# Kernel optimization log

Measured on AMD Instinct MI355X. Metric: run time of the kernel, lower is better.

The kernel has to match this reference:

```python
import jax, jax.numpy as jnp
import numpy as np

B, L, D_MODEL, N_HEADS = 2, 2048, 2048, 16
HALF = D_MODEL // 2            # 1024
HD = HALF // N_HEADS           # 64 (head dim actually used by the reshape)
SCALE = float(np.sqrt(D_MODEL / N_HEADS))  # sqrt(128), per source's self.scale
EPS = 1e-5


def setup_inputs() -> dict:
    key = jax.random.key(0)
    ks = jax.random.split(key, 12)
    s = 1.0 / np.sqrt(HALF)
    d = dict(
        x_a=jax.random.normal(ks[0], (B, L, HALF), jnp.float32),
        x_b=jax.random.normal(ks[1], (B, L, HALF), jnp.float32),
        Wq_a=jax.random.normal(ks[2], (HALF, HALF), jnp.float32) * s,
        Wq_b=jax.random.normal(ks[3], (HALF, HALF), jnp.float32) * s,
        Wk_a=jax.random.normal(ks[4], (HALF, HALF), jnp.float32) * s,
        Wk_b=jax.random.normal(ks[5], (HALF, HALF), jnp.float32) * s,
        Wv_a=jax.random.normal(ks[6], (HALF, HALF), jnp.float32) * s,
        Wv_b=jax.random.normal(ks[7], (HALF, HALF), jnp.float32) * s,
        Wo_a=jax.random.normal(ks[8], (HALF, HALF), jnp.float32) * s,
        Wo_b=jax.random.normal(ks[9], (HALF, HALF), jnp.float32) * s,
        gamma_a=jnp.ones((HALF,), jnp.float32),
        beta_a=jnp.zeros((HALF,), jnp.float32),
        gamma_b=jnp.ones((HALF,), jnp.float32),
        beta_b=jnp.zeros((HALF,), jnp.float32),
    )
    return d


def _heads(x, W):
    # torch Linear (no bias): x @ W.T, then split heads -> (B, H, L, HD)
    y = jnp.einsum('bld,ed->ble', x, W)
    Bb, Ll, _ = y.shape
    return y.reshape(Bb, Ll, N_HEADS, HD).transpose(0, 2, 1, 3)


def _ln(x, gamma, beta):
    mu = jnp.mean(x, axis=-1, keepdims=True)
    var = jnp.var(x, axis=-1, keepdims=True)
    return (x - mu) * jax.lax.rsqrt(var + EPS) * gamma + beta


def reference(x_a, x_b, Wq_a, Wq_b, Wk_a, Wk_b, Wv_a, Wv_b, Wo_a, Wo_b,
              gamma_a, beta_a, gamma_b, beta_b):
    q_a = _heads(x_a, Wq_a); k_a = _heads(x_a, Wk_a); v_a = _heads(x_a, Wv_a)
    q_b = _heads(x_b, Wq_b); k_b = _heads(x_b, Wk_b); v_b = _heads(x_b, Wv_b)

    # cross-attention: branch a attends over branch b and vice versa
    scores_a = jnp.einsum('bhqd,bhkd->bhqk', q_a, k_b) / SCALE
    scores_b = jnp.einsum('bhqd,bhkd->bhqk', q_b, k_a) / SCALE
    w_a = jax.nn.softmax(scores_a, axis=-1)
    w_b = jax.nn.softmax(scores_b, axis=-1)

    o_a = jnp.einsum('bhqk,bhkd->bhqd', w_a, v_b)
    o_b = jnp.einsum('bhqk,bhkd->bhqd', w_b, v_a)
    o_a = o_a.transpose(0, 2, 1, 3).reshape(x_a.shape)
    o_b = o_b.transpose(0, 2, 1, 3).reshape(x_b.shape)

    o_a = jnp.einsum('bld,ed->ble', o_a, Wo_a)
    o_b = jnp.einsum('bld,ed->ble', o_b, Wo_b)

    y_a = _ln(x_a + o_a, gamma_a, beta_a)
    y_b = _ln(x_b + o_b, gamma_b, beta_b)
    return y_a, y_b
```

## Files before the change

### kernel.cpp

```cpp
#include <hip/hip_runtime.h>
#include <cstdint>
#include <cstddef>

typedef __bf16 bf16x8 __attribute__((ext_vector_type(8)));
typedef float f32x4 __attribute__((ext_vector_type(4)));
typedef unsigned short u16x8 __attribute__((ext_vector_type(8)));
typedef unsigned short u16x4 __attribute__((ext_vector_type(4)));
typedef short s16x4 __attribute__((ext_vector_type(4)));
typedef unsigned short u16;

#define L_SEQ 2048
#define D_HALF 1024
#define HDIM 64
static constexpr float EXP2_SCALE = 0.12751742552639395f;

__device__ inline u16 f2b(float f) {
  uint32_t u; __builtin_memcpy(&u, &f, 4);
  u = u + 0x7FFFu + ((u >> 16) & 1u);
  return (u16)(u >> 16);
}

__device__ inline uint32_t cvt_pk_bf16(float lo, float hi) {
  uint32_t r;
  asm("v_cvt_pk_bf16_f32 %0, %1, %2" : "=v"(r) : "v"(lo), "v"(hi));
  return r;
}

#define GLOAD16(gp, lp) __builtin_amdgcn_global_load_lds( \
    (const __attribute__((address_space(1))) unsigned int*)(gp), \
    (__attribute__((address_space(3))) unsigned int*)(lp), 16, 0, 0)

struct CArgAll { const float* src[10]; u16* dst[10]; };
__global__ __launch_bounds__(256)
void convall(CArgAll a) {
  const int id = blockIdx.x;
  const float* s; u16* d; int blk;
  if (id < 4096) { int p = id >> 11; blk = id & 2047; s = a.src[p]; d = a.dst[p]; }
  else { int w = (id - 4096) >> 9; blk = (id - 4096) & 511; s = a.src[2 + w]; d = a.dst[2 + w]; }
  size_t i = ((size_t)blk * 256 + threadIdx.x) * 8;
  float4 v0 = *(const float4*)(s + i);
  float4 v1 = *(const float4*)(s + i + 4);
  u16x8 p;
  p[0] = f2b(v0.x); p[1] = f2b(v0.y); p[2] = f2b(v0.z); p[3] = f2b(v0.w);
  p[4] = f2b(v1.x); p[5] = f2b(v1.y); p[6] = f2b(v1.z); p[7] = f2b(v1.w);
  *(u16x8*)&d[i] = p;
}

struct GArg { const u16* A; const u16* W; u16* C; const float* R; float* Z;
              int vt; float alpha; };
struct GArgs { GArg g[6]; };

template <bool RESID>
__global__ __launch_bounds__(256)
void gemm_nt(GArgs args, int M, int N, int K) {
  GArg ga = args.g[blockIdx.z];
  __shared__ __attribute__((aligned(16))) u16 As[2][8192];
  __shared__ __attribute__((aligned(16))) u16 Bs[2][8192];

  const int tid = threadIdx.x;
  const int wv = tid >> 6, lane = tid & 63;
  const int lane15 = lane & 15, quad = lane >> 4;
  const int m0 = blockIdx.y * 128, n0 = blockIdx.x * 128;
  const int wm = (wv >> 1) * 64, wn = (wv & 1) * 64;

  const int srow = lane >> 3;
  const int scol = ((lane & 7) ^ srow) * 8;

  const u16* pA[4]; const u16* pW[4]; int lo[4];
#pragma unroll
  for (int j = 0; j < 4; j++) {
    int r = wv * 32 + j * 8;
    pA[j] = ga.A + (size_t)(m0 + r + srow) * K + scol;
    pW[j] = ga.W + (size_t)(n0 + r + srow) * K + scol;
    lo[j] = r * 64;
  }

  f32x4 acc[4][4] = {};
  const int swz = (lane15 & 7) << 4;
  const int NT = K >> 6;

#pragma unroll
  for (int j = 0; j < 4; j++) {
    GLOAD16(pA[j], &As[0][lo[j]]);
    GLOAD16(pW[j], &Bs[0][lo[j]]);
  }
#pragma unroll
  for (int j = 0; j < 4; j++) {
    GLOAD16(pA[j] + 64, &As[1][lo[j]]);
    GLOAD16(pW[j] + 64, &Bs[1][lo[j]]);
  }
  asm volatile("s_waitcnt vmcnt(8)" ::: "memory");
  __builtin_amdgcn_s_barrier();
  __builtin_amdgcn_sched_barrier(0);

  for (int t = 0; t < NT; ++t) {
    const int cur = t & 1;
    const char* ab = (const char*)As[cur];
    const char* bb = (const char*)Bs[cur];
#pragma unroll
    for (int kk = 0; kk < 2; kk++) {
      const int cb = kk * 64 + quad * 16;
      bf16x8 af[4], bw[4];
#pragma unroll
      for (int i = 0; i < 4; i++)
        af[i] = *(const bf16x8*)(ab + (wm + i * 16 + lane15) * 128 + (cb ^ swz));
#pragma unroll
      for (int j = 0; j < 4; j++)
        bw[j] = *(const bf16x8*)(bb + (wn + j * 16 + lane15) * 128 + (cb ^ swz));
#pragma unroll
      for (int i = 0; i < 4; i++)
#pragma unroll
        for (int j = 0; j < 4; j++)
          acc[i][j] = __builtin_amdgcn_mfma_f32_16x16x32_bf16(af[i], bw[j], acc[i][j], 0, 0, 0);
    }
    __builtin_amdgcn_sched_barrier(0);
    __builtin_amdgcn_s_barrier();
    __builtin_amdgcn_sched_barrier(0);
    if (t + 2 < NT) {
#pragma unroll
      for (int j = 0; j < 4; j++) {
        GLOAD16(pA[j] + (size_t)(t + 2) * 64, &As[cur][lo[j]]);
        GLOAD16(pW[j] + (size_t)(t + 2) * 64, &Bs[cur][lo[j]]);
      }
      asm volatile("s_waitcnt vmcnt(8)" ::: "memory");
    } else if (t + 1 < NT) {
      asm volatile("s_waitcnt vmcnt(0)" ::: "memory");
    }
    if (t + 1 < NT) {
      __builtin_amdgcn_s_barrier();
      __builtin_amdgcn_sched_barrier(0);
    }
  }

  const float al = ga.alpha;
  if (!RESID && ga.vt) {
#pragma unroll
    for (int i = 0; i < 4; i++)
#pragma unroll
      for (int j = 0; j < 4; j++) {
        int gm0 = m0 + wm + i * 16 + quad * 4;
        int gn  = n0 + wn + j * 16 + lane15;
        int bb2 = gm0 >> 11, tt = gm0 & 2047;
        u16x4 pk;
#pragma unroll
        for (int r = 0; r < 4; r++) pk[r] = f2b(acc[i][j][r] * al);
        *(u16x4*)&ga.C[(size_t)bb2 * 2097152 + (size_t)gn * 2048 + tt] = pk;
      }
  } else {
#pragma unroll
    for (int i = 0; i < 4; i++)
#pragma unroll
      for (int j = 0; j < 4; j++)
#pragma unroll
        for (int r = 0; r < 4; r++) {
          int gm = m0 + wm + i * 16 + quad * 4 + r;
          int gn = n0 + wn + j * 16 + lane15;
          size_t idx = (size_t)gm * N + gn;
          if (RESID) ga.Z[idx] = acc[i][j][r] + ga.R[idx];
          else       ga.C[idx] = f2b(acc[i][j][r] * al);
        }
  }
}

#define SWZ(row, bcol) ((row) * 128 + ((bcol) ^ (((row) & 7) << 4)))

__global__ __launch_bounds__(256, 2)
void attn_kernel(const u16* q_a, const u16* k_a, const u16* vt_a,
                 const u16* q_b, const u16* k_b, const u16* vt_b,
                 u16* o_a, u16* o_b) {
  const int br = blockIdx.z;
  const u16* Q  = br ? q_b : q_a;
  const u16* Kp = br ? k_a : k_b;
  const u16* Vp = br ? vt_a : vt_b;
  u16* O = br ? o_b : o_a;
  const int bh = blockIdx.y;
  const int b = bh >> 4, h = bh & 15;
  const int q0 = blockIdx.x * 128;

  const int tid = threadIdx.x, wv = tid >> 6, lane = tid & 63;
  const int lane15 = lane & 15, quad = lane >> 4;

  __shared__ __attribute__((aligned(16))) u16 Ks[2][4096];
  __shared__ __attribute__((aligned(16))) u16 Vt[2][4096];

  const size_t base   = ((size_t)b * L_SEQ) * D_HALF + (size_t)h * HDIM;
  const size_t vbase  = (size_t)b * 2097152 + (size_t)(h * 64) * 2048;

  const int c1 = tid + 256;
  const int r0 = tid >> 3, cb0 = (tid & 7) * 16;
  const int r1 = c1 >> 3,  cb1 = (c1 & 7) * 16;
  const int wo0 = SWZ(r0, cb0), wo1 = SWZ(r1, cb1);

  bf16x8 qf[2][2];
#pragma unroll
  for (int f = 0; f < 2; f++) {
    const int qrow = q0 + wv * 32 + f * 16 + lane15;
#pragma unroll
    for (int c = 0; c < 2; c++)
      qf[f][c] = *(const bf16x8*)&Q[base + (size_t)qrow * D_HALF + c * 32 + quad * 8];
  }

  u16x8 kr0 = *(const u16x8*)&Kp[base + (size_t)r0 * D_HALF + cb0 / 2];
  u16x8 kr1 = *(const u16x8*)&Kp[base + (size_t)r1 * D_HALF + cb1 / 2];
  u16x8 vr0 = *(const u16x8*)&Vp[vbase + (size_t)r0 * 2048 + cb0 / 2];
  u16x8 vr1 = *(const u16x8*)&Vp[vbase + (size_t)r1 * 2048 + cb1 / 2];
  *(u16x8*)((char*)Ks[0] + wo0) = kr0;
  *(u16x8*)((char*)Ks[0] + wo1) = kr1;
  *(u16x8*)((char*)Vt[0] + wo0) = vr0;
  *(u16x8*)((char*)Vt[0] + wo1) = vr1;
  __syncthreads();

  f32x4 oacc[2][4] = {};
  float lsum[2] = {0.f, 0.f};

  for (int it = 0; it < 32; it++) {
    const int cur = it & 1, nxt = cur ^ 1;
    if (it < 31) {
      const int kt = (it + 1) * 64;
      kr0 = *(const u16x8*)&Kp[base + (size_t)(kt + r0) * D_HALF + cb0 / 2];
      kr1 = *(const u16x8*)&Kp[base + (size_t)(kt + r1) * D_HALF + cb1 / 2];
      vr0 = *(const u16x8*)&Vp[vbase + (size_t)r0 * 2048 + kt + cb0 / 2];
      vr1 = *(const u16x8*)&Vp[vbase + (size_t)r1 * 2048 + kt + cb1 / 2];
    }

    const char* kb = (const char*)Ks[cur];
    const char* vb = (const char*)Vt[cur];

    f32x4 s[2][4];
    __builtin_amdgcn_s_setprio(1);
#pragma unroll
    for (int nt = 0; nt < 4; nt++) {
      const int krow = nt * 16 + lane15;
      bf16x8 kb0 = *(const bf16x8*)(kb + SWZ(krow, quad * 16));
      bf16x8 kb1 = *(const bf16x8*)(kb + SWZ(krow, 64 + quad * 16));
#pragma unroll
      for (int f = 0; f < 2; f++) {
        f32x4 a0 = {};
        a0 = __builtin_amdgcn_mfma_f32_16x16x32_bf16(kb0, qf[f][0], a0, 0, 0, 0);
        a0 = __builtin_amdgcn_mfma_f32_16x16x32_bf16(kb1, qf[f][1], a0, 0, 0, 0);
        s[f][nt] = a0;
      }
    }
    __builtin_amdgcn_s_setprio(0);

    s16x4 pa[2][4];
#pragma unroll
    for (int f = 0; f < 2; f++)
#pragma unroll
      for (int nt = 0; nt < 4; nt++) {
        float p0 = __builtin_amdgcn_exp2f(s[f][nt][0]);
        float p1 = __builtin_amdgcn_exp2f(s[f][nt][1]);
        float p2 = __builtin_amdgcn_exp2f(s[f][nt][2]);
        float p3 = __builtin_amdgcn_exp2f(s[f][nt][3]);
        lsum[f] += (p0 + p1) + (p2 + p3);
        union { uint32_t u[2]; s16x4 v; } cv;
        cv.u[0] = cvt_pk_bf16(p0, p1);
        cv.u[1] = cvt_pk_bf16(p2, p3);
        pa[f][nt] = cv.v;
      }

    __builtin_amdgcn_s_setprio(1);
#pragma unroll
    for (int dt = 0; dt < 4; dt++) {
      const int vrow = dt * 16 + lane15;
      s16x4 bv[4];
#pragma unroll
      for (int nt = 0; nt < 4; nt++)
        bv[nt] = *(const s16x4*)(vb + SWZ(vrow, nt * 32 + quad * 8));
#pragma unroll
      for (int f = 0; f < 2; f++) {
        f32x4 t = oacc[f][dt];
#pragma unroll
        for (int nt = 0; nt < 4; nt++)
          t = __builtin_amdgcn_mfma_f32_16x16x16bf16_1k(pa[f][nt], bv[nt], t, 0, 0, 0);
        oacc[f][dt] = t;
      }
    }
    __builtin_amdgcn_s_setprio(0);

    if (it < 31) {
      *(u16x8*)((char*)Ks[nxt] + wo0) = kr0;
      *(u16x8*)((char*)Ks[nxt] + wo1) = kr1;
      *(u16x8*)((char*)Vt[nxt] + wo0) = vr0;
      *(u16x8*)((char*)Vt[nxt] + wo1) = vr1;
    }
    __syncthreads();
  }

#pragma unroll
  for (int f = 0; f < 2; f++) {
    float lt = lsum[f];
    lt += __shfl_xor(lt, 16);
    lt += __shfl_xor(lt, 32);
    lsum[f] = lt;
  }
#pragma unroll
  for (int f = 0; f < 2; f++) {
    float linv[4];
#pragma unroll
    for (int r = 0; r < 4; r++)
      linv[r] = 1.0f / __shfl(lsum[f], quad * 4 + r);
#pragma unroll
    for (int dt = 0; dt < 4; dt++)
#pragma unroll
      for (int r = 0; r < 4; r++) {
        float val = oacc[f][dt][r] * linv[r];
        O[base + (size_t)(q0 + wv * 32 + f * 16 + quad * 4 + r) * D_HALF
          + dt * 16 + lane15] = f2b(val);
      }
  }
}

__global__ __launch_bounds__(256)
void ln_kernel(const float* zA, const float* zB,
               const float* gA, const float* bA, const float* gB, const float* bB,
               float* out) {
  const int row = blockIdx.x, br = blockIdx.y;
  const float* z = (br ? zB : zA) + (size_t)row * D_HALF;
  const float* g  = br ? gB : gA;
  const float* be = br ? bB : bA;
  float* o = out + (size_t)br * ((size_t)4096 * D_HALF) + (size_t)row * D_HALF;

  float4 v = ((const float4*)z)[threadIdx.x];
  float s  = v.x + v.y + v.z + v.w;
  float s2 = v.x * v.x + v.y * v.y + v.z * v.z + v.w * v.w;
#pragma unroll
  for (int off = 32; off > 0; off >>= 1) {
    s  += __shfl_down(s, off);
    s2 += __shfl_down(s2, off);
  }
  __shared__ float red[8];
  int w = threadIdx.x >> 6, ln = threadIdx.x & 63;
  if (ln == 0) { red[w] = s; red[4 + w] = s2; }
  __syncthreads();
  if (threadIdx.x == 0) {
    red[0] = red[0] + red[1] + red[2] + red[3];
    red[4] = red[4] + red[5] + red[6] + red[7];
  }
  __syncthreads();
  float mu  = red[0] * (1.0f / 1024.0f);
  float var = red[4] * (1.0f / 1024.0f) - mu * mu;
  float rs  = rsqrtf(fmaxf(var, 0.0f) + 1e-5f);

  int col = threadIdx.x * 4;
  float4 gv = ((const float4*)g)[threadIdx.x];
  float4 bv = ((const float4*)be)[threadIdx.x];
  float4 ov;
  ov.x = (v.x - mu) * rs * gv.x + bv.x;
  ov.y = (v.y - mu) * rs * gv.y + bv.y;
  ov.z = (v.z - mu) * rs * gv.z + bv.z;
  ov.w = (v.w - mu) * rs * gv.w + bv.w;
  *(float4*)&o[col] = ov;
}

extern "C" void kernel_launch(void* const* d_in, const int* in_sizes, int n_in,
                              void* d_out, int out_size, void* d_ws, size_t ws_size,
                              hipStream_t stream) {
  const float* x_a     = (const float*)d_in[0];
  const float* x_b     = (const float*)d_in[1];
  const float* Wq_a    = (const float*)d_in[2];
  const float* Wq_b    = (const float*)d_in[3];
  const float* Wk_a    = (const float*)d_in[4];
  const float* Wk_b    = (const float*)d_in[5];
  const float* Wv_a    = (const float*)d_in[6];
  const float* Wv_b    = (const float*)d_in[7];
  const float* Wo_a    = (const float*)d_in[8];
  const float* Wo_b    = (const float*)d_in[9];
  const float* gamma_a = (const float*)d_in[10];
  const float* beta_a  = (const float*)d_in[11];
  const float* gamma_b = (const float*)d_in[12];
  const float* beta_b  = (const float*)d_in[13];

  const size_t BUF = (size_t)4096 * 1024;
  u16* ws   = (u16*)d_ws;
  u16* q_a  = ws + 0 * BUF; u16* k_a  = ws + 1 * BUF; u16* vt_a = ws + 2 * BUF;
  u16* q_b  = ws + 3 * BUF; u16* k_b  = ws + 4 * BUF; u16* vt_b = ws + 5 * BUF;
  u16* wall = ws + 6 * BUF;
  float* z_a = (float*)(ws + 0 * BUF);
  float* z_b = (float*)(ws + 2 * BUF);

  u16* xbf_a = (u16*)d_out;
  u16* xbf_b = xbf_a + 4194304;
  u16* o_a   = (u16*)d_out;
  u16* o_b   = o_a + 4194304;

  const int M = 4096, N = 1024, K = 1024;

  CArgAll ca;
  ca.src[0] = x_a;  ca.dst[0] = xbf_a;
  ca.src[1] = x_b;  ca.dst[1] = xbf_b;
  ca.src[2] = Wq_a; ca.src[3] = Wk_a; ca.src[4] = Wv_a;
  ca.src[5] = Wq_b; ca.src[6] = Wk_b; ca.src[7] = Wv_b;
  ca.src[8] = Wo_a; ca.src[9] = Wo_b;
  for (int w = 0; w < 8; w++) ca.dst[2 + w] = wall + (size_t)w * 1048576;
  convall<<<dim3(8192), 256, 0, stream>>>(ca);

  GArgs qkv;
  qkv.g[0] = GArg{xbf_a, wall + 0 * 1048576, q_a,  nullptr, nullptr, 0, EXP2_SCALE};
  qkv.g[1] = GArg{xbf_a, wall + 1 * 1048576, k_a,  nullptr, nullptr, 0, 1.0f};
  qkv.g[2] = GArg{xbf_a, wall + 2 * 1048576, vt_a, nullptr, nullptr, 1, 1.0f};
  qkv.g[3] = GArg{xbf_b, wall + 3 * 1048576, q_b,  nullptr, nullptr, 0, EXP2_SCALE};
  qkv.g[4] = GArg{xbf_b, wall + 4 * 1048576, k_b,  nullptr, nullptr, 0, 1.0f};
  qkv.g[5] = GArg{xbf_b, wall + 5 * 1048576, vt_b, nullptr, nullptr, 1, 1.0f};
  gemm_nt<false><<<dim3(8, 32, 6), 256, 0, stream>>>(qkv, M, N, K);

  attn_kernel<<<dim3(16, 32, 2), 256, 0, stream>>>(q_a, k_a, vt_a, q_b, k_b, vt_b, o_a, o_b);

  GArgs op;
  op.g[0] = GArg{o_a, wall + 6 * 1048576, nullptr, x_a, z_a, 0, 1.0f};
  op.g[1] = GArg{o_b, wall + 7 * 1048576, nullptr, x_b, z_b, 0, 1.0f};
  op.g[2] = op.g[0]; op.g[3] = op.g[0]; op.g[4] = op.g[0]; op.g[5] = op.g[0];
  gemm_nt<true><<<dim3(8, 32, 2), 256, 0, stream>>>(op, M, N, K);

  ln_kernel<<<dim3(4096, 2), 256, 0, stream>>>(z_a, z_b, gamma_a, beta_a,
                                               gamma_b, beta_b, (float*)d_out);
}
```

Measured before the change: 342.0 us.

## Single-buffer GEMM LDS and remap 1D grid with XCD-aware block swizzle

Replaces the hand-scheduled double-buffered LDS pipeline in the NT GEMM with a simple single-buffer load/sync/compute loop. This halves LDS use so more workgroups can fit per CU. It also flattens the launch grid to 1D and remaps block ids so consecutive ids land on the same XCD, interleaving the GEMM sub-problems (z) for better L2 locality. The cost is that global loads no longer overlap with MFMA compute, so each k-step now waits for its loads behind two barriers.

```diff
diff --git a/kernel.cpp b/kernel.cpp
--- a/kernel.cpp
+++ b/kernel.cpp
@@ -52,15 +52,23 @@
 
 template <bool RESID>
 __global__ __launch_bounds__(256)
-void gemm_nt(GArgs args, int M, int N, int K) {
-  GArg ga = args.g[blockIdx.z];
-  __shared__ __attribute__((aligned(16))) u16 As[2][8192];
-  __shared__ __attribute__((aligned(16))) u16 Bs[2][8192];
+void gemm_nt(GArgs args, int N, int K, int ZN) {
+  const int nwg = gridDim.x;
+  const int q8 = nwg >> 3;
+  const int bid = ((int)blockIdx.x & 7) * q8 + ((int)blockIdx.x >> 3);
+  const int z = bid % ZN;
+  const int rem = bid / ZN;
+  const int nx = N >> 7;
+  const int bx = rem % nx, by = rem / nx;
+
+  GArg ga = args.g[z];
+  __shared__ __attribute__((aligned(16))) u16 As[8192];
+  __shared__ __attribute__((aligned(16))) u16 Bs[8192];
 
   const int tid = threadIdx.x;
   const int wv = tid >> 6, lane = tid & 63;
   const int lane15 = lane & 15, quad = lane >> 4;
-  const int m0 = blockIdx.y * 128, n0 = blockIdx.x * 128;
+  const int m0 = by * 128, n0 = bx * 128;
   const int wm = (wv >> 1) * 64, wn = (wv & 1) * 64;
 
   const int srow = lane >> 3;
@@ -77,26 +85,17 @@
 
   f32x4 acc[4][4] = {};
   const int swz = (lane15 & 7) << 4;
-  const int NT = K >> 6;
-
-#pragma unroll
-  for (int j = 0; j < 4; j++) {
-    GLOAD16(pA[j], &As[0][lo[j]]);
-    GLOAD16(pW[j], &Bs[0][lo[j]]);
-  }
-#pragma unroll
-  for (int j = 0; j < 4; j++) {
-    GLOAD16(pA[j] + 64, &As[1][lo[j]]);
-    GLOAD16(pW[j] + 64, &Bs[1][lo[j]]);
-  }
-  asm volatile("s_waitcnt vmcnt(8)" ::: "memory");
-  __builtin_amdgcn_s_barrier();
-  __builtin_amdgcn_sched_barrier(0);
-
-  for (int t = 0; t < NT; ++t) {
-    const int cur = t & 1;
-    const char* ab = (const char*)As[cur];
-    const char* bb = (const char*)Bs[cur];
+
+  for (int k0 = 0; k0 < K; k0 += 64) {
+    __syncthreads();
+#pragma unroll
+    for (int j = 0; j < 4; j++) {
+      GLOAD16(pA[j] + k0, &As[lo[j]]);
+      GLOAD16(pW[j] + k0, &Bs[lo[j]]);
+    }
+    __syncthreads();
+    const char* ab = (const char*)As;
+    const char* bb = (const char*)Bs;
 #pragma unroll
     for (int kk = 0; kk < 2; kk++) {
       const int cb = kk * 64 + quad * 16;
@@ -112,23 +111,6 @@
 #pragma unroll
         for (int j = 0; j < 4; j++)
           acc[i][j] = __builtin_amdgcn_mfma_f32_16x16x32_bf16(af[i], bw[j], acc[i][j], 0, 0, 0);
-    }
-    __builtin_amdgcn_sched_barrier(0);
-    __builtin_amdgcn_s_barrier();
-    __builtin_amdgcn_sched_barrier(0);
-    if (t + 2 < NT) {
-#pragma unroll
-      for (int j = 0; j < 4; j++) {
-        GLOAD16(pA[j] + (size_t)(t + 2) * 64, &As[cur][lo[j]]);
-        GLOAD16(pW[j] + (size_t)(t + 2) * 64, &Bs[cur][lo[j]]);
-      }
-      asm volatile("s_waitcnt vmcnt(8)" ::: "memory");
-    } else if (t + 1 < NT) {
-      asm volatile("s_waitcnt vmcnt(0)" ::: "memory");
-    }
-    if (t + 1 < NT) {
-      __builtin_amdgcn_s_barrier();
-      __builtin_amdgcn_sched_barrier(0);
     }
   }
 
@@ -384,7 +366,7 @@
   u16* o_a   = (u16*)d_out;
   u16* o_b   = o_a + 4194304;
 
-  const int M = 4096, N = 1024, K = 1024;
+  const int N = 1024, K = 1024;
 
   CArgAll ca;
   ca.src[0] = x_a;  ca.dst[0] = xbf_a;
@@ -402,7 +384,7 @@
   qkv.g[3] = GArg{xbf_b, wall + 3 * 1048576, q_b,  nullptr, nullptr, 0, EXP2_SCALE};
   qkv.g[4] = GArg{xbf_b, wall + 4 * 1048576, k_b,  nullptr, nullptr, 0, 1.0f};
   qkv.g[5] = GArg{xbf_b, wall + 5 * 1048576, vt_b, nullptr, nullptr, 1, 1.0f};
-  gemm_nt<false><<<dim3(8, 32, 6), 256, 0, stream>>>(qkv, M, N, K);
+  gemm_nt<false><<<dim3(8 * 32 * 6), 256, 0, stream>>>(qkv, N, K, 6);
 
   attn_kernel<<<dim3(16, 32, 2), 256, 0, stream>>>(q_a, k_a, vt_a, q_b, k_b, vt_b, o_a, o_b);
 
@@ -410,7 +392,7 @@
   op.g[0] = GArg{o_a, wall + 6 * 1048576, nullptr, x_a, z_a, 0, 1.0f};
   op.g[1] = GArg{o_b, wall + 7 * 1048576, nullptr, x_b, z_b, 0, 1.0f};
   op.g[2] = op.g[0]; op.g[3] = op.g[0]; op.g[4] = op.g[0]; op.g[5] = op.g[0];
-  gemm_nt<true><<<dim3(8, 32, 2), 256, 0, stream>>>(op, M, N, K);
+  gemm_nt<true><<<dim3(8 * 32 * 2), 256, 0, stream>>>(op, N, K, 2);
 
   ln_kernel<<<dim3(4096, 2), 256, 0, stream>>>(z_a, z_b, gamma_a, beta_a,
                                                gamma_b, beta_b, (float*)d_out);
```

After: 341.7 us. Within noise of the previous version (-0.1%).
